# Optimization experiments

Measured on AMD Instinct MI355X. Metric: run time of the kernel, lower is better.

Reference implementation:

```python
import jax, jax.numpy as jnp
import numpy as np

B, S, D, H = 4, 2048, 1024, 16
HD = D // H  # head_dim = 64


def setup_inputs() -> dict:
    key = jax.random.key(0)
    ks = jax.random.split(key, 5)
    scale = 1.0 / np.sqrt(D)  # xavier-ish
    return {
        "query": jax.random.normal(ks[0], (B, S, D), dtype=jnp.float32),
        "Wq": jax.random.normal(ks[1], (D, D), dtype=jnp.float32) * scale,
        "bq": jnp.zeros((D,), dtype=jnp.float32),
        "Wk": jax.random.normal(ks[2], (D, D), dtype=jnp.float32) * scale,
        "bk": jnp.zeros((D,), dtype=jnp.float32),
        "Wv": jax.random.normal(ks[3], (D, D), dtype=jnp.float32) * scale,
        "bv": jnp.zeros((D,), dtype=jnp.float32),
        "Wo": jax.random.normal(ks[4], (D, D), dtype=jnp.float32) * scale,
        "bo": jnp.zeros((D,), dtype=jnp.float32),
    }


def reference(query, Wq, bq, Wk, bk, Wv, bv, Wo, bo):
    # Self-attention: key = value = query. Linear layers use y = x @ W^T + b (torch nn.Linear).
    q = query @ Wq.T + bq
    k = query @ Wk.T + bk
    v = query @ Wv.T + bv
    # [B, S, D] -> [B, H, S, HD]
    q = q.reshape(B, S, H, HD).transpose(0, 2, 1, 3)
    k = k.reshape(B, S, H, HD).transpose(0, 2, 1, 3)
    v = v.reshape(B, S, H, HD).transpose(0, 2, 1, 3)
    scores = jnp.einsum('bhqd,bhkd->bhqk', q, k) / jnp.sqrt(jnp.float32(HD))
    attn = jax.nn.softmax(scores, axis=-1)  # dropout=0 (eval)
    out = jnp.einsum('bhqk,bhkd->bhqd', attn, v)
    out = out.transpose(0, 2, 1, 3).reshape(B, S, D)
    out = out @ Wo.T + bo
    return out
```

## Files before the change

kernel.cpp:

```cpp
#include <hip/hip_runtime.h>
#include <cstdint>


#define B_ 4
#define S_ 2048
#define D_ 1024
#define H_ 16
#define HD_ 64
#define QKV_N 3072
#define QK_LD 2048
#define SCALE_Q 0.18033688011111772f

typedef __bf16 bf16x8 __attribute__((ext_vector_type(8)));
typedef __bf16 bf16x2 __attribute__((ext_vector_type(2)));
typedef float f32x4 __attribute__((ext_vector_type(4)));
typedef short short8 __attribute__((ext_vector_type(8)));

__device__ __forceinline__ unsigned short f2bf(float f) {
  unsigned int u = __builtin_bit_cast(unsigned int, f);
  u = (u + 0x7FFFu + ((u >> 16) & 1u)) >> 16;
  return (unsigned short)u;
}

__device__ __forceinline__ unsigned int pkbf(float a, float b) {
  bf16x2 v;
  v.x = (__bf16)a;
  v.y = (__bf16)b;
  return __builtin_bit_cast(unsigned int, v);
}

__device__ __forceinline__ void gload16(const void* g, void* l) {
  __builtin_amdgcn_global_load_lds(
      (const __attribute__((address_space(1))) void*)g,
      (__attribute__((address_space(3))) void*)l, 16, 0, 0);
}

__global__ __launch_bounds__(256) void cvt_bf16(const float* __restrict__ in,
                                                unsigned short* __restrict__ out, int n8) {
  int i = blockIdx.x * 256 + threadIdx.x;
  if (i >= n8) return;
  const float4* p = (const float4*)in + (size_t)i * 2;
  float4 a = p[0], b = p[1];
  unsigned short o[8] = {f2bf(a.x), f2bf(a.y), f2bf(a.z), f2bf(a.w),
                         f2bf(b.x), f2bf(b.y), f2bf(b.z), f2bf(b.w)};
  *(uint4*)(out + (size_t)i * 8) = *(const uint4*)o;
}

__global__ __launch_bounds__(256) void cvt_w4(const float* __restrict__ w0, const float* __restrict__ w1,
                                              const float* __restrict__ w2, const float* __restrict__ w3,
                                              unsigned short* __restrict__ dst) {
  int y = blockIdx.y;
  const float* src = (y == 0) ? w0 : (y == 1) ? w1 : (y == 2) ? w2 : w3;
  float s = (y == 0) ? SCALE_Q : 1.0f;
  int i = blockIdx.x * 256 + threadIdx.x;
  const float4* p = (const float4*)src + (size_t)i * 2;
  float4 a = p[0], b = p[1];
  unsigned short o[8] = {f2bf(a.x * s), f2bf(a.y * s), f2bf(a.z * s), f2bf(a.w * s),
                         f2bf(b.x * s), f2bf(b.y * s), f2bf(b.z * s), f2bf(b.w * s)};
  *(uint4*)(dst + (size_t)y * 1048576 + (size_t)i * 8) = *(const uint4*)o;
}

__global__ __launch_bounds__(256) void bias_cat(const float* __restrict__ bq, const float* __restrict__ bk,
                                                const float* __restrict__ bv, float* __restrict__ bcat) {
  int i = blockIdx.x * 256 + threadIdx.x;
  float v = (i < 1024) ? bq[i] * SCALE_Q : (i < 2048) ? bk[i - 1024] : bv[i - 2048];
  bcat[i] = v;
}

__global__ __launch_bounds__(256) void gemm_bt(
    const unsigned short* __restrict__ A, const unsigned short* __restrict__ W,
    const float* __restrict__ bias, void* __restrict__ Cout,
    unsigned short* __restrict__ vt, int M, int N, int K, int mode) {
  __shared__ __attribute__((aligned(16))) unsigned short sA[128 * 32];
  __shared__ __attribute__((aligned(16))) unsigned short sB[128 * 32];
  const int t = threadIdx.x;
  const int lane = t & 63;
  const int w = t >> 6;
  const int lm = lane & 15;
  const int quad = lane >> 4;
  const int m0 = blockIdx.x * 128;
  const int n0 = blockIdx.y * 128;
  const int wm = (w & 1) * 64;
  const int wn = (w >> 1) * 64;

  const int off0 = t * 8, off1 = t * 8 + 2048;
  const int ar0 = off0 >> 5, ac0 = (((off0 >> 3) & 3) ^ ((ar0 >> 1) & 3)) * 8;
  const int ar1 = off1 >> 5, ac1 = (((off1 >> 3) & 3) ^ ((ar1 >> 1) & 3)) * 8;
  const unsigned short* Ag0 = A + (size_t)(m0 + ar0) * K + ac0;
  const unsigned short* Ag1 = A + (size_t)(m0 + ar1) * K + ac1;
  const unsigned short* Wg0 = W + (size_t)(n0 + ar0) * K + ac0;
  const unsigned short* Wg1 = W + (size_t)(n0 + ar1) * K + ac1;
  unsigned short* sA0 = &sA[w * 512];
  unsigned short* sA1 = &sA[2048 + w * 512];
  unsigned short* sB0 = &sB[w * 512];
  unsigned short* sB1 = &sB[2048 + w * 512];

  f32x4 acc[4][4] = {};

  for (int kt = 0; kt < K; kt += 32) {
    gload16(Ag0 + kt, sA0);
    gload16(Ag1 + kt, sA1);
    gload16(Wg0 + kt, sB0);
    gload16(Wg1 + kt, sB1);
    __syncthreads();
    bf16x8 af[4], bf[4];
#pragma unroll
    for (int mi = 0; mi < 4; ++mi) {
      int row = wm + mi * 16 + lm;
      af[mi] = *(const bf16x8*)&sA[row * 32 + ((quad ^ ((row >> 1) & 3)) << 3)];
    }
#pragma unroll
    for (int ni = 0; ni < 4; ++ni) {
      int row = wn + ni * 16 + lm;
      bf[ni] = *(const bf16x8*)&sB[row * 32 + ((quad ^ ((row >> 1) & 3)) << 3)];
    }
#pragma unroll
    for (int mi = 0; mi < 4; ++mi)
#pragma unroll
      for (int ni = 0; ni < 4; ++ni)
        acc[mi][ni] = __builtin_amdgcn_mfma_f32_16x16x32_bf16(af[mi], bf[ni], acc[mi][ni], 0, 0, 0);
    __syncthreads();
  }

#pragma unroll
  for (int mi = 0; mi < 4; ++mi)
#pragma unroll
    for (int ni = 0; ni < 4; ++ni) {
      int col = n0 + wn + ni * 16 + lm;
      float bv = bias[col];
      float v0 = acc[mi][ni][0] + bv, v1 = acc[mi][ni][1] + bv;
      float v2 = acc[mi][ni][2] + bv, v3 = acc[mi][ni][3] + bv;
      int rbase = m0 + wm + mi * 16 + quad * 4;
      if (mode == 0) {
        float* op = (float*)Cout;
        op[(size_t)(rbase + 0) * N + col] = v0;
        op[(size_t)(rbase + 1) * N + col] = v1;
        op[(size_t)(rbase + 2) * N + col] = v2;
        op[(size_t)(rbase + 3) * N + col] = v3;
      } else if (col < 2048) {
        unsigned short* op = (unsigned short*)Cout;
        op[(size_t)(rbase + 0) * QK_LD + col] = f2bf(v0);
        op[(size_t)(rbase + 1) * QK_LD + col] = f2bf(v1);
        op[(size_t)(rbase + 2) * QK_LD + col] = f2bf(v2);
        op[(size_t)(rbase + 3) * QK_LD + col] = f2bf(v3);
      } else {
        int c = col - 2048;
        int bh = (m0 >> 11) * 16 + (c >> 6);
        int hd = c & 63;
        int sbase = (rbase & 2047);
        uint2 pk = {pkbf(v0, v1), pkbf(v2, v3)};
        *(uint2*)(vt + (size_t)bh * (HD_ * S_) + (size_t)hd * S_ + sbase) = pk;
      }
    }
}

__global__ __launch_bounds__(256, 2) void attn_kernel(
    const unsigned short* __restrict__ qk, const unsigned short* __restrict__ vt,
    unsigned short* __restrict__ ab) {
  __shared__ __attribute__((aligned(16))) unsigned short sK[2][64 * 64];
  __shared__ __attribute__((aligned(16))) unsigned short sV[2][64 * 64];
  __shared__ __attribute__((aligned(16))) unsigned short sP[4][64 * 64];

  const int t = threadIdx.x;
  const int lane = t & 63;
  const int w = t >> 6;
  const int lm = lane & 15;
  const int quad = lane >> 4;
  const int bh = blockIdx.x & 63;
  const int b = bh >> 4, h = bh & 15;
  const int q0 = (blockIdx.x >> 6) * 256;

  const unsigned short* qg = qk + (size_t)b * S_ * QK_LD + h * HD_;
  const unsigned short* kg = qg + 1024;
  const unsigned short* vg = vt + (size_t)bh * HD_ * S_;

  const int off0 = t * 8, off1 = off0 + 2048;
  const int r0 = off0 >> 6, c0 = (((off0 >> 3) & 7) ^ (r0 & 7)) * 8;
  const int r1 = off1 >> 6, c1 = (((off1 >> 3) & 7) ^ (r1 & 7)) * 8;

  gload16(kg + (size_t)r0 * QK_LD + c0, &sK[0][w * 512]);
  gload16(kg + (size_t)r1 * QK_LD + c1, &sK[0][2048 + w * 512]);
  gload16(vg + (size_t)r0 * S_ + c0, &sV[0][w * 512]);
  gload16(vg + (size_t)r1 * S_ + c1, &sV[0][2048 + w * 512]);

  bf16x8 qf[4][2];
#pragma unroll
  for (int mi = 0; mi < 4; ++mi) {
    int row = q0 + w * 64 + mi * 16 + lm;
#pragma unroll
    for (int kc = 0; kc < 2; ++kc)
      qf[mi][kc] = *(const bf16x8*)(qg + (size_t)row * QK_LD + kc * 32 + quad * 8);
  }
  __syncthreads();

  unsigned short* sPw = sP[w];
  const bf16x8 ones = __builtin_bit_cast(bf16x8, (short8)(short)0x3F80);
  f32x4 o[4][4] = {};
  f32x4 Lacc[4] = {};

  for (int n0 = 0; n0 < S_; n0 += 64) {
    const int cur = (n0 >> 6) & 1, nxt = cur ^ 1;
    if (n0 + 64 < S_) {
      gload16(kg + (size_t)(n0 + 64 + r0) * QK_LD + c0, &sK[nxt][w * 512]);
      gload16(kg + (size_t)(n0 + 64 + r1) * QK_LD + c1, &sK[nxt][2048 + w * 512]);
      gload16(vg + (size_t)r0 * S_ + (n0 + 64) + c0, &sV[nxt][w * 512]);
      gload16(vg + (size_t)r1 * S_ + (n0 + 64) + c1, &sV[nxt][2048 + w * 512]);
    }

    f32x4 s[4][4] = {};
#pragma unroll
    for (int kc = 0; kc < 2; ++kc)
#pragma unroll
      for (int nb = 0; nb < 4; ++nb) {
        int row = nb * 16 + lm;
        bf16x8 kf = *(const bf16x8*)&sK[cur][row * 64 + (((kc * 4 + quad) ^ (row & 7)) << 3)];
#pragma unroll
        for (int mi = 0; mi < 4; ++mi)
          s[mi][nb] = __builtin_amdgcn_mfma_f32_16x16x32_bf16(kf, qf[mi][kc], s[mi][nb], 0, 0, 0);
      }

#pragma unroll
    for (int mi = 0; mi < 4; ++mi) {
      int prow = mi * 16 + lm;
      char* rowp = (char*)sPw + prow * 128;
#pragma unroll
      for (int nb = 0; nb < 4; ++nb) {
        const f32x4& sv = s[mi][nb];
        uint2 pk = {pkbf(__builtin_amdgcn_exp2f(sv[0]), __builtin_amdgcn_exp2f(sv[1])),
                    pkbf(__builtin_amdgcn_exp2f(sv[2]), __builtin_amdgcn_exp2f(sv[3]))};
        int c16 = (nb * 2 + (quad >> 1)) ^ (prow & 7);
        *(uint2*)(rowp + (c16 << 4) + ((quad & 1) << 3)) = pk;
      }
    }

#pragma unroll
    for (int kc = 0; kc < 2; ++kc) {
      bf16x8 pf[4];
#pragma unroll
      for (int mi = 0; mi < 4; ++mi) {
        int prow = mi * 16 + lm;
        pf[mi] = *(const bf16x8*)&sPw[prow * 64 + (((kc * 4 + quad) ^ (prow & 7)) << 3)];
        Lacc[mi] = __builtin_amdgcn_mfma_f32_16x16x32_bf16(pf[mi], ones, Lacc[mi], 0, 0, 0);
      }
#pragma unroll
      for (int nf = 0; nf < 4; ++nf) {
        int row = nf * 16 + lm;
        bf16x8 vf = *(const bf16x8*)&sV[cur][row * 64 + (((kc * 4 + quad) ^ (row & 7)) << 3)];
#pragma unroll
        for (int mi = 0; mi < 4; ++mi)
          o[mi][nf] = __builtin_amdgcn_mfma_f32_16x16x32_bf16(pf[mi], vf, o[mi][nf], 0, 0, 0);
      }
    }
    __syncthreads();
  }

#pragma unroll
  for (int mi = 0; mi < 4; ++mi)
#pragma unroll
    for (int r = 0; r < 4; ++r) {
      float rinv = 1.0f / Lacc[mi][r];
      int row = q0 + w * 64 + mi * 16 + quad * 4 + r;
#pragma unroll
      for (int nf = 0; nf < 4; ++nf) {
        int col = h * HD_ + nf * 16 + lm;
        ab[(size_t)(b * S_ + row) * D_ + col] = f2bf(o[mi][nf][r] * rinv);
      }
    }
}

extern "C" void kernel_launch(void* const* d_in, const int* in_sizes, int n_in,
                              void* d_out, int out_size, void* d_ws, size_t ws_size,
                              hipStream_t stream) {
  const float* x = (const float*)d_in[0];
  const float* Wq = (const float*)d_in[1];
  const float* bq = (const float*)d_in[2];
  const float* Wk = (const float*)d_in[3];
  const float* bk = (const float*)d_in[4];
  const float* Wv = (const float*)d_in[5];
  const float* bv = (const float*)d_in[6];
  const float* Wo = (const float*)d_in[7];
  const float* bo = (const float*)d_in[8];
  float* out = (float*)d_out;

  const size_t E = (size_t)B_ * S_ * D_;
  const size_t WE = (size_t)D_ * D_;
  unsigned short* xb = (unsigned short*)d_ws;
  unsigned short* wcat = xb + E;
  unsigned short* wob = wcat + 3 * WE;
  float* bcat = (float*)(wcat + 4 * WE);
  unsigned short* qkb = (unsigned short*)(bcat + 4096);
  unsigned short* vtb = qkb + (size_t)B_ * S_ * QK_LD;
  unsigned short* abuf = xb;

  cvt_bf16<<<dim3((unsigned)(E / 8 / 256)), 256, 0, stream>>>(x, xb, (int)(E / 8));
  cvt_w4<<<dim3(512, 4), 256, 0, stream>>>(Wq, Wk, Wv, Wo, wcat);
  bias_cat<<<dim3(12), 256, 0, stream>>>(bq, bk, bv, bcat);

  gemm_bt<<<dim3((B_ * S_) / 128, QKV_N / 128), 256, 0, stream>>>(
      xb, wcat, bcat, qkb, vtb, B_ * S_, QKV_N, D_, 1);
  attn_kernel<<<dim3(512), 256, 0, stream>>>(qkb, vtb, abuf);
  gemm_bt<<<dim3((B_ * S_) / 128, D_ / 128), 256, 0, stream>>>(
      abuf, wob, bo, out, nullptr, B_ * S_, D_, D_, 0);
}
```

Baseline: 273.9 us.

## Add 256x256-tile pipelined QKV GEMM kernel with XCD-aware block mapping

Replaces the generic 128x128 QKV projection GEMM with a dedicated 512-thread kernel that computes 256x256 output tiles. It uses double-buffered swizzled LDS, direct global-to-LDS loads interleaved with MFMA phases, and setprio hints. Blocks are remapped so that neighbouring M tiles land on the same XCD, which should improve L2 reuse. The aim is higher arithmetic intensity and hiding load latency, at the cost of 128KB of LDS per block, heavy register use, and complex hand scheduling that may limit occupancy.

```diff
diff --git a/kernel.cpp b/kernel.cpp
--- a/kernel.cpp
+++ b/kernel.cpp
@@ -65,6 +65,161 @@
   int i = blockIdx.x * 256 + threadIdx.x;
   float v = (i < 1024) ? bq[i] * SCALE_Q : (i < 2048) ? bk[i - 1024] : bv[i - 2048];
   bcat[i] = v;
+}
+
+
+__device__ __forceinline__ void ld_afrag(const unsigned short* s, int rowbase, int quad,
+                                         int sw, bf16x8 af[4][2]) {
+#pragma unroll
+  for (int mi2 = 0; mi2 < 4; ++mi2) {
+    int row = rowbase + mi2 * 16;
+#pragma unroll
+    for (int kk = 0; kk < 2; ++kk)
+      af[mi2][kk] = *(const bf16x8*)&s[row * 64 + ((((kk << 2) + quad) ^ sw) << 3)];
+  }
+}
+
+__device__ __forceinline__ void ld_bfrag(const unsigned short* s, int rowbase, int quad,
+                                         int sw, bf16x8 bf[2][2]) {
+#pragma unroll
+  for (int ni2 = 0; ni2 < 2; ++ni2) {
+    int row = rowbase + ni2 * 16;
+#pragma unroll
+    for (int kk = 0; kk < 2; ++kk)
+      bf[ni2][kk] = *(const bf16x8*)&s[row * 64 + ((((kk << 2) + quad) ^ sw) << 3)];
+  }
+}
+
+#define SBAR() __builtin_amdgcn_sched_barrier(0)
+#define BARRIER()                      \
+  do {                                 \
+    SBAR();                            \
+    __builtin_amdgcn_s_barrier();      \
+    SBAR();                            \
+  } while (0)
+#define WAITLGKM()                                      \
+  do {                                                  \
+    asm volatile("s_waitcnt lgkmcnt(0)" ::: "memory");  \
+    SBAR();                                             \
+  } while (0)
+
+#define MM(qm, qn, BF)                                                                   \
+  _Pragma("unroll") for (int mi2 = 0; mi2 < 4; ++mi2)                                    \
+  _Pragma("unroll") for (int ni2 = 0; ni2 < 2; ++ni2)                                    \
+  _Pragma("unroll") for (int kk = 0; kk < 2; ++kk)                                       \
+      acc[(qm) * 4 + mi2][(qn) * 2 + ni2] = __builtin_amdgcn_mfma_f32_16x16x32_bf16(     \
+          af[mi2][kk], BF[ni2][kk], acc[(qm) * 4 + mi2][(qn) * 2 + ni2], 0, 0, 0);
+
+__global__ __launch_bounds__(512, 2) void gemm_qkv_256(
+    const unsigned short* __restrict__ A, const unsigned short* __restrict__ W,
+    const float* __restrict__ bias, unsigned short* __restrict__ qk,
+    unsigned short* __restrict__ vt) {
+  __shared__ __attribute__((aligned(16))) unsigned short sA[2][256 * 64];
+  __shared__ __attribute__((aligned(16))) unsigned short sB[2][256 * 64];
+
+  const int t = threadIdx.x;
+  const int lane = t & 63;
+  const int w = t >> 6;
+  const int lm = lane & 15;
+  const int quad = lane >> 4;
+  const int sw = lm & 7;
+  const int wm = (w >> 2) * 128;
+  const int wn = (w & 3) * 64;
+
+  const int bid = blockIdx.x;
+  const int xcd = bid & 7, lin = bid >> 3;
+  const int mt = xcd * 4 + (lin & 3);
+  const int nt = lin >> 2;
+  const int m0 = mt * 256, n0 = nt * 256;
+  const int K = 1024;
+
+  const int srow = t >> 3;
+  const int scol = ((t & 7) ^ ((t >> 3) & 7)) << 3;
+  const unsigned short* Ab = A + ((size_t)m0 + srow) * K + scol;
+  const unsigned short* Wb = W + ((size_t)n0 + srow) * K + scol;
+
+#define STG_A(bb, q, kt) gload16(Ab + (size_t)((q) * 64) * K + (kt), &sA[bb][(q) * 4096 + w * 512])
+#define STG_B(bb, q, kt) gload16(Wb + (size_t)((q) * 64) * K + (kt), &sB[bb][(q) * 4096 + w * 512])
+
+  STG_A(0, 0, 0); STG_A(0, 1, 0); STG_A(0, 2, 0); STG_A(0, 3, 0);
+  STG_B(0, 0, 0); STG_B(0, 1, 0); STG_B(0, 2, 0); STG_B(0, 3, 0);
+  STG_A(1, 0, 64); STG_A(1, 2, 64);
+  STG_B(1, 0, 64); STG_B(1, 1, 64);
+  STG_A(1, 1, 64); STG_A(1, 3, 64);
+  asm volatile("s_waitcnt vmcnt(6)" ::: "memory");
+  BARRIER();
+
+  f32x4 acc[8][4] = {};
+  bf16x8 af[4][2], bf0[2][2], bf1[2][2];
+
+#define GROUP(c, kn1, kn2)                                                            \
+  do {                                                                                \
+                                                              \
+    ld_afrag(sA[c], wm + lm, quad, sw, af);                                           \
+    ld_bfrag(sB[c], wn + lm, quad, sw, bf0);                                          \
+    STG_B(c ^ 1, 2, kn1);                                                             \
+    STG_B(c ^ 1, 3, kn1);                                                             \
+    BARRIER(); WAITLGKM();                                                            \
+    __builtin_amdgcn_s_setprio(1); MM(0, 0, bf0); __builtin_amdgcn_s_setprio(0);      \
+    BARRIER();                                                                        \
+                                                              \
+    ld_bfrag(sB[c], wn + 32 + lm, quad, sw, bf1);                                     \
+    STG_A(c, 0, kn2);                                                                 \
+    STG_A(c, 2, kn2);                                                                 \
+    BARRIER(); WAITLGKM();                                                            \
+    __builtin_amdgcn_s_setprio(1); MM(0, 1, bf1); __builtin_amdgcn_s_setprio(0);      \
+    BARRIER();                                                                        \
+                                                              \
+    ld_afrag(sA[c], wm + 64 + lm, quad, sw, af);                                      \
+    STG_B(c, 0, kn2);                                                                 \
+    STG_B(c, 1, kn2);                                                                 \
+    BARRIER(); WAITLGKM();                                                            \
+    __builtin_amdgcn_s_setprio(1); MM(1, 0, bf0); __builtin_amdgcn_s_setprio(0);      \
+    BARRIER();                                                                        \
+                                                              \
+    STG_A(c, 1, kn2);                                                                 \
+    STG_A(c, 3, kn2);                                                                 \
+    asm volatile("s_waitcnt vmcnt(6)" ::: "memory");                                  \
+    BARRIER();                                                                        \
+    __builtin_amdgcn_s_setprio(1); MM(1, 1, bf1); __builtin_amdgcn_s_setprio(0);      \
+    BARRIER();                                                                        \
+  } while (0)
+
+  for (int kt = 0; kt < K; kt += 128) {
+    const int kn1a = kt + 64;
+    const int kn2a = (kt + 128 < K) ? kt + 128 : K - 64;
+    const int kn1b = kn2a;
+    const int kn2b = (kt + 192 < K) ? kt + 192 : K - 64;
+    GROUP(0, kn1a, kn2a);
+    GROUP(1, kn1b, kn2b);
+  }
+
+  asm volatile("s_waitcnt vmcnt(0)" ::: "memory");
+
+#pragma unroll
+  for (int mi = 0; mi < 8; ++mi) {
+    const int rbase = m0 + wm + mi * 16 + quad * 4;
+#pragma unroll
+    for (int ni = 0; ni < 4; ++ni) {
+      const int col = n0 + wn + ni * 16 + lm;
+      const float bv = bias[col];
+      float v0 = acc[mi][ni][0] + bv, v1 = acc[mi][ni][1] + bv;
+      float v2 = acc[mi][ni][2] + bv, v3 = acc[mi][ni][3] + bv;
+      if (n0 < 2048) {
+        qk[(size_t)(rbase + 0) * QK_LD + col] = f2bf(v0);
+        qk[(size_t)(rbase + 1) * QK_LD + col] = f2bf(v1);
+        qk[(size_t)(rbase + 2) * QK_LD + col] = f2bf(v2);
+        qk[(size_t)(rbase + 3) * QK_LD + col] = f2bf(v3);
+      } else {
+        int c = col - 2048;
+        int bh = (m0 >> 11) * 16 + (c >> 6);
+        int hd = c & 63;
+        int sbase = rbase & 2047;
+        uint2 pk = {pkbf(v0, v1), pkbf(v2, v3)};
+        *(uint2*)(vt + (size_t)bh * (HD_ * S_) + (size_t)hd * S_ + sbase) = pk;
+      }
+    }
+  }
 }
 
 __global__ __launch_bounds__(256) void gemm_bt(
@@ -296,8 +451,7 @@
   cvt_w4<<<dim3(512, 4), 256, 0, stream>>>(Wq, Wk, Wv, Wo, wcat);
   bias_cat<<<dim3(12), 256, 0, stream>>>(bq, bk, bv, bcat);
 
-  gemm_bt<<<dim3((B_ * S_) / 128, QKV_N / 128), 256, 0, stream>>>(
-      xb, wcat, bcat, qkb, vtb, B_ * S_, QKV_N, D_, 1);
+  gemm_qkv_256<<<dim3(384), 512, 0, stream>>>(xb, wcat, bcat, qkb, vtb);
   attn_kernel<<<dim3(512), 256, 0, stream>>>(qkb, vtb, abuf);
   gemm_bt<<<dim3((B_ * S_) / 128, D_ / 128), 256, 0, stream>>>(
       abuf, wob, bo, out, nullptr, B_ * S_, D_, D_, 0);
```

After: 277.4 us. No clear change (+1.3%).
